# Performance work log

Hardware: AMD Instinct MI355X
Metric: run time of the kernel (lower is better)

## Reference

```python
import jax, jax.numpy as jnp
import numpy as np
from jax import lax

EPS = 1e-5
CARD = 32


def _bn(x, gamma, beta):
    # training-mode BatchNorm2d: batch statistics over (N, H, W) per channel
    mean = jnp.mean(x, axis=(0, 2, 3), keepdims=True)
    var = jnp.var(x, axis=(0, 2, 3), keepdims=True)
    inv = lax.rsqrt(var + EPS)
    return gamma[None, :, None, None] * (x - mean) * inv + beta[None, :, None, None]


def _conv(x, w, stride=1, padding='VALID', groups=1):
    return lax.conv_general_dilated(
        x, w, window_strides=(stride, stride), padding=padding,
        dimension_numbers=('NCHW', 'OIHW', 'NCHW'),
        feature_group_count=groups)


def setup_inputs() -> dict:
    key = jax.random.key(0)
    ks = jax.random.split(key, 4)
    N, Cin, H, W = 32, 256, 56, 56
    D, Cout = 16, 256
    CD = CARD * D  # 512
    x = jax.random.normal(ks[0], (N, Cin, H, W), dtype=jnp.float32)
    w1 = jax.random.normal(ks[1], (CD, Cin, 1, 1), dtype=jnp.float32) * 0.05
    w3 = jax.random.normal(ks[2], (CD, D, 3, 3), dtype=jnp.float32) * 0.05
    wa = jax.random.normal(ks[3], (Cout, CD, 1, 1), dtype=jnp.float32) * 0.05
    return {
        'x': x,
        'w1': w1, 'g1': jnp.ones(CD), 'b1': jnp.zeros(CD),
        'w3': w3, 'g3': jnp.ones(CD), 'b3': jnp.zeros(CD),
        'wa': wa, 'ga': jnp.ones(Cout), 'ba': jnp.zeros(Cout),
    }


def reference(x, w1, g1, b1, w3, g3, b3, wa, ga, ba):
    # 32 paths of (1x1 conv -> BN -> ReLU -> 3x3 conv -> BN -> ReLU) then concat
    # is exactly: one 1x1 conv to 512ch -> BN -> ReLU -> grouped 3x3 conv (32 groups)
    # -> BN -> ReLU  (per-channel BN commutes with channel concatenation).
    out = _conv(x, w1)                                   # [N, 512, H, W]
    out = jax.nn.relu(_bn(out, g1, b1))
    out = _conv(out, w3, stride=1, padding=((1, 1), (1, 1)), groups=CARD)
    out = jax.nn.relu(_bn(out, g3, b3))
    out = _conv(out, wa)                                 # [N, 256, H, W]
    out = _bn(out, ga, ba)
    out = out + x                                        # identity shortcut (stride=1, Cin==Cout)
    return jax.nn.relu(out)
```

## Files before the change

### kernel.cpp

```cpp
#include <hip/hip_runtime.h>

#define HW 3136
#define NPOS 100352.0f
#define NSLICE 32

typedef unsigned short ushortT;
typedef __attribute__((ext_vector_type(8))) short short8;
typedef __attribute__((ext_vector_type(4))) float floatx4;

__device__ inline float bf2f(ushortT u) {
    union { unsigned int i; float f; } v; v.i = ((unsigned int)u) << 16; return v.f;
}
__device__ inline ushortT f2bf(float f) {
    union { float f; unsigned int i; } v; v.f = f;
    unsigned int r = v.i + 0x7FFFu + ((v.i >> 16) & 1u);
    return (ushortT)(r >> 16);
}
__device__ inline unsigned int cvtpk(float lo, float hi) {
    unsigned int r;
    asm("v_cvt_pk_bf16_f32 %0, %1, %2" : "=v"(r) : "v"(lo), "v"(hi));
    return r;
}

__device__ inline void gl_lds16(const ushortT* g, ushortT* l) {
    __builtin_amdgcn_global_load_lds(
        (const __attribute__((address_space(1))) unsigned int*)g,
        (__attribute__((address_space(3))) unsigned int*)l, 16, 0, 0);
}

__global__ __launch_bounds__(256) void prep_k(const float* __restrict__ w1,
                                              const float* __restrict__ w3,
                                              const float* __restrict__ wa,
                                              ushortT* __restrict__ w1b,
                                              ushortT* __restrict__ wab,
                                              ushortT* __restrict__ w3b,
                                              float* __restrict__ partials) {
    int i = blockIdx.x * 256 + threadIdx.x;
    if (i < 131072) { w1b[i] = f2bf(w1[i]); wab[i] = f2bf(wa[i]); }
    if (i < 81920) {
        int ic = i & 15, oc = (i >> 4) & 15, rest = i >> 8;
        int s = rest % 10, g = rest / 10;
        w3b[i] = (s < 9) ? f2bf(w3[(((g * 16 + oc) * 16) + ic) * 9 + s]) : (ushortT)0;
        partials[i] = 0.f;
    }
}

__global__ __launch_bounds__(256) void transx_k(const float* __restrict__ x,
                                                ushortT* __restrict__ xb) {
    __shared__ float tf[64 * 65];
    const int t = threadIdx.x;
    const int p0 = blockIdx.x * 64, k0 = blockIdx.y * 64, n = blockIdx.z;
#pragma unroll
    for (int i = 0; i < 16; i++) {
        int idx = t + i * 256;
        int k = idx >> 6, p = idx & 63;
        tf[k * 65 + p] = x[((size_t)n * 256 + k0 + k) * HW + p0 + p];
    }
    __syncthreads();
#pragma unroll
    for (int i = 0; i < 2; i++) {
        int idx = t + i * 256;
        int p = idx >> 3, kq = (idx & 7) * 8;
        short8 o;
#pragma unroll
        for (int j = 0; j < 8; j++) o[j] = (short)f2bf(tf[(kq + j) * 65 + p]);
        *(short8*)&xb[((size_t)n * HW + p0 + p) * 256 + k0 + kq] = o;
    }
}

__global__ __launch_bounds__(512) void gemm1_k(const ushortT* __restrict__ xb,
                                               const ushortT* __restrict__ w1b,
                                               const float* __restrict__ zpad,
                                               ushortT* __restrict__ t1,
                                               float* __restrict__ p1) {
    __shared__ ushortT As[128 * 64];
    __shared__ ushortT Bs[256 * 64];
    const int t = threadIdx.x;
    const int P0 = blockIdx.x * 256, C0 = blockIdx.y * 128, n = blockIdx.z;
    const int w = t >> 6, lane = t & 63;
    const int mh = (w >> 2) * 64, nh = (w & 3) * 64;
    const int l15 = lane & 15, quad = lane >> 4;

    const int lrow = lane >> 3;
    const int slin = lane & 7;

    const ushortT* agp[2];
#pragma unroll
    for (int i = 0; i < 2; i++) {
        int row = w * 16 + lrow + i * 8;
        int sl = (slin ^ (row & 7)) * 8;
        agp[i] = w1b + (size_t)(C0 + row) * 256 + sl;
    }
    const ushortT* bgp[4];
#pragma unroll
    for (int i = 0; i < 4; i++) {
        int row = w * 32 + lrow + i * 8;
        int sl = (slin ^ (row & 7)) * 8;
        int p = P0 + row;
        bgp[i] = (p < HW) ? xb + ((size_t)n * HW + p) * 256 + sl
                          : (const ushortT*)zpad;
    }
    ushortT* al = As + (w * 16) * 64;
    ushortT* bl = Bs + (w * 32) * 64;

    floatx4 acc[4][4];
#pragma unroll
    for (int a = 0; a < 4; a++)
#pragma unroll
        for (int b = 0; b < 4; b++)
#pragma unroll
            for (int e = 0; e < 4; e++) acc[a][b][e] = 0.f;

    for (int kb = 0; kb < 256; kb += 64) {
#pragma unroll
        for (int i = 0; i < 2; i++) gl_lds16(agp[i] + kb, al + i * 512);
#pragma unroll
        for (int i = 0; i < 4; i++) gl_lds16(bgp[i] + kb, bl + i * 512);
        __syncthreads();
#pragma unroll
        for (int ks = 0; ks < 2; ks++) {
            short8 af[4], bfv[4];
#pragma unroll
            for (int mt = 0; mt < 4; mt++) {
                int row = mh + mt * 16 + l15, rx = row & 7;
                af[mt] = *(const short8*)&As[row * 64 + (((ks * 4 + quad) ^ rx) * 8)];
            }
#pragma unroll
            for (int nt = 0; nt < 4; nt++) {
                int row = nh + nt * 16 + l15, rx = row & 7;
                bfv[nt] = *(const short8*)&Bs[row * 64 + (((ks * 4 + quad) ^ rx) * 8)];
            }
#pragma unroll
            for (int mt = 0; mt < 4; mt++)
#pragma unroll
                for (int nt = 0; nt < 4; nt++)
                    acc[mt][nt] = __builtin_amdgcn_mfma_f32_16x16x32_bf16(
                        af[mt], bfv[nt], acc[mt][nt], 0, 0, 0);
        }
        __syncthreads();
    }
#pragma unroll
    for (int mt = 0; mt < 4; mt++) {
        int c = C0 + mh + mt * 16 + quad * 4;
#pragma unroll
        for (int nt = 0; nt < 4; nt++) {
            int pp = P0 + nh + nt * 16 + l15;
            if (pp < HW) {
                ushort4 o;
                o.x = f2bf(acc[mt][nt][0]); o.y = f2bf(acc[mt][nt][1]);
                o.z = f2bf(acc[mt][nt][2]); o.w = f2bf(acc[mt][nt][3]);
                *(ushort4*)&t1[((size_t)n * HW + pp) * 512 + c] = o;
            }
        }
    }
    float* ps = p1 + ((blockIdx.x + blockIdx.z * 13) & (NSLICE - 1)) * 1024;
#pragma unroll
    for (int mt = 0; mt < 4; mt++) {
        int c = C0 + mh + mt * 16 + quad * 4;
#pragma unroll
        for (int e = 0; e < 4; e++) {
            float sv = acc[mt][0][e] + acc[mt][1][e] + acc[mt][2][e] + acc[mt][3][e];
            float qv = acc[mt][0][e] * acc[mt][0][e] + acc[mt][1][e] * acc[mt][1][e]
                     + acc[mt][2][e] * acc[mt][2][e] + acc[mt][3][e] * acc[mt][3][e];
            sv += __shfl_xor(sv, 1); qv += __shfl_xor(qv, 1);
            sv += __shfl_xor(sv, 2); qv += __shfl_xor(qv, 2);
            sv += __shfl_xor(sv, 4); qv += __shfl_xor(qv, 4);
            sv += __shfl_xor(sv, 8); qv += __shfl_xor(qv, 8);
            if (l15 == 0) {
                atomicAdd(&ps[c + e], sv);
                atomicAdd(&ps[512 + c + e], qv);
            }
        }
    }
}

__global__ __launch_bounds__(256) void gconv_k(const ushortT* __restrict__ t1,
                                               const ushortT* __restrict__ w3b,
                                               const float* __restrict__ p1,
                                               const float* __restrict__ g1,
                                               const float* __restrict__ b1,
                                               ushortT* __restrict__ t2,
                                               float* __restrict__ p2) {
    __shared__ ushortT tile[8 * 590 * 8];
    __shared__ float scs[64], shs[64];
    const int t = threadIdx.x;
    const int rt = blockIdx.x, gg = blockIdx.y, n = blockIdx.z;
    const int r0 = rt * 8;

    if (t < 64) {
        int c = gg * 64 + t;
        float S = 0.f, Q = 0.f;
#pragma unroll
        for (int s = 0; s < NSLICE; s++) {
            S += p1[s * 1024 + c];
            Q += p1[s * 1024 + 512 + c];
        }
        float m = S * (1.f / NPOS);
        float var = Q * (1.f / NPOS) - m * m;
        float sc = g1[c] * rsqrtf(var + 1e-5f);
        scs[t] = sc; shs[t] = b1[c] - m * sc;
    }
    __syncthreads();

    const int chq = t & 7;
    float sc8[8], sh8[8];
#pragma unroll
    for (int j = 0; j < 8; j++) { sc8[j] = scs[chq * 8 + j]; sh8[j] = shs[chq * 8 + j]; }

    const ushortT* src = t1 + (size_t)n * HW * 512 + gg * 64 + chq * 8;
    short8 vreg[19];
#pragma unroll
    for (int i = 0; i < 19; i++) {
        int idx = t + i * 256;
        int pos = idx >> 3;
        int row = pos / 58, col = pos - row * 58;
        int ir = r0 - 1 + row, icl = col - 1;
        if (idx < 4640 && ir >= 0 && ir < 56 && icl >= 0 && icl < 56)
            vreg[i] = *(const short8*)&src[(size_t)(ir * 56 + icl) * 512];
    }
#pragma unroll
    for (int i = 0; i < 19; i++) {
        int idx = t + i * 256;
        if (idx >= 4640) continue;
        int pos = idx >> 3;
        int row = pos / 58, col = pos - row * 58;
        int ir = r0 - 1 + row, icl = col - 1;
        short8 o;
        if (ir >= 0 && ir < 56 && icl >= 0 && icl < 56) {
            float f[8];
#pragma unroll
            for (int j = 0; j < 8; j++)
                f[j] = fmaxf(fmaf(sc8[j], bf2f((ushortT)vreg[i][j]), sh8[j]), 0.f);
            union { short8 s; unsigned int u[4]; } ov;
#pragma unroll
            for (int j = 0; j < 4; j++) ov.u[j] = cvtpk(f[2 * j], f[2 * j + 1]);
            o = ov.s;
        } else {
#pragma unroll
            for (int j = 0; j < 8; j++) o[j] = 0;
        }
        *(short8*)&tile[((chq * 590) + row * 59 + col) * 8] = o;
    }
    __syncthreads();

    const int w = t >> 6, lane = t & 63;
    const int l15 = lane & 15, quad = lane >> 4;
    const int qh = quad >> 1, ql = quad & 1;
    const int g = gg * 4 + w;

    short8 af[5];
    int drv[5], dcv[5];
#pragma unroll
    for (int s = 0; s < 5; s++) {
        int shift = 2 * s + qh;
        af[s] = *(const short8*)&w3b[((g * 10 + shift) * 16 + l15) * 16 + ql * 8];
        if (shift == 9) shift = 8;
        drv[s] = shift / 3; dcv[s] = shift - drv[s] * 3;
    }

    const int pr = l15 >> 2, pc = l15 & 3;
    const int plane = (w * 2 + ql) * 590;
    float s4[4] = {0.f, 0.f, 0.f, 0.f}, q4[4] = {0.f, 0.f, 0.f, 0.f};

#pragma unroll
    for (int rh = 0; rh < 2; rh++) {
        const int rbase = rh * 4 + pr;
        floatx4 acc[14];
#pragma unroll
        for (int ct = 0; ct < 14; ct++)
#pragma unroll
            for (int e = 0; e < 4; e++) acc[ct][e] = 0.f;

#pragma unroll
        for (int ct = 0; ct < 14; ct++) {
            int colb = ct * 4 + pc;
#pragma unroll
            for (int s = 0; s < 5; s++) {
                short8 bfv = *(const short8*)&tile[(plane + (rbase + drv[s]) * 59 + colb + dcv[s]) * 8];
                acc[ct] = __builtin_amdgcn_mfma_f32_16x16x32_bf16(af[s], bfv, acc[ct], 0, 0, 0);
            }
        }
#pragma unroll
        for (int ct = 0; ct < 14; ct++) {
            int pos = (r0 + rh * 4 + pr) * 56 + ct * 4 + pc;
            ushort4 o;
            o.x = f2bf(acc[ct][0]); o.y = f2bf(acc[ct][1]);
            o.z = f2bf(acc[ct][2]); o.w = f2bf(acc[ct][3]);
            *(ushort4*)&t2[((size_t)n * HW + pos) * 512 + g * 16 + quad * 4] = o;
#pragma unroll
            for (int e = 0; e < 4; e++) {
                float a = acc[ct][e];
                s4[e] += a; q4[e] += a * a;
            }
        }
    }
    float* ps = p2 + ((blockIdx.x + blockIdx.z * 7) & (NSLICE - 1)) * 1024;
#pragma unroll
    for (int e = 0; e < 4; e++) {
        float sv = s4[e], qv = q4[e];
        sv += __shfl_xor(sv, 1); qv += __shfl_xor(qv, 1);
        sv += __shfl_xor(sv, 2); qv += __shfl_xor(qv, 2);
        sv += __shfl_xor(sv, 4); qv += __shfl_xor(qv, 4);
        sv += __shfl_xor(sv, 8); qv += __shfl_xor(qv, 8);
        if (l15 == 0) {
            atomicAdd(&ps[g * 16 + quad * 4 + e], sv);
            atomicAdd(&ps[512 + g * 16 + quad * 4 + e], qv);
        }
    }
}

__global__ __launch_bounds__(512) void gemm3_k(const ushortT* __restrict__ t2,
                                               const ushortT* __restrict__ wab,
                                               const float* __restrict__ p2,
                                               const float* __restrict__ g3,
                                               const float* __restrict__ b3,
                                               ushortT* __restrict__ t3,
                                               float* __restrict__ p3) {
    __shared__ ushortT As[256 * 64];
    __shared__ ushortT Bs[128 * 64];
    __shared__ float2 scsh[512];
    const int t = threadIdx.x;
    const int P0 = blockIdx.x * 128, n = blockIdx.y;
    const int w = t >> 6, lane = t & 63;
    const int mh = (w >> 1) * 64, nh = (w & 1) * 64;
    const int l15 = lane & 15, quad = lane >> 4;
    const int slin = t & 7;

    int brow[2]; const ushortT* bgp[2]; bool bval[2];
#pragma unroll
    for (int i = 0; i < 2; i++) {
        int row = (t >> 3) + i * 64;
        brow[i] = row;
        int p = P0 + row;
        bval[i] = (p < HW);
        int pe = bval[i] ? p : (HW - 1);
        bgp[i] = t2 + ((size_t)n * HW + pe) * 512 + slin * 8;
    }
    const int srow = w * 32 + (lane >> 3);
    const ushortT* agp[4];
#pragma unroll
    for (int i = 0; i < 4; i++) {
        int row = srow + i * 8;
        int sl = ((lane & 7) ^ (row & 7)) * 8;
        agp[i] = wab + (size_t)row * 512 + sl;
    }
    ushortT* al = As + (w * 32) * 64;

    short8 breg[2];
#pragma unroll
    for (int i = 0; i < 2; i++) breg[i] = *(const short8*)(bgp[i]);

    {
        int c = t;
        float S = 0.f, Q = 0.f;
#pragma unroll
        for (int s = 0; s < NSLICE; s++) {
            S += p2[s * 1024 + c];
            Q += p2[s * 1024 + 512 + c];
        }
        float m = S * (1.f / NPOS);
        float var = Q * (1.f / NPOS) - m * m;
        float sc = g3[c] * rsqrtf(var + 1e-5f);
        scsh[c] = make_float2(sc, b3[c] - m * sc);
    }
    __syncthreads();

    floatx4 acc[4][4];
#pragma unroll
    for (int a = 0; a < 4; a++)
#pragma unroll
        for (int b = 0; b < 4; b++)
#pragma unroll
            for (int e = 0; e < 4; e++) acc[a][b][e] = 0.f;

    for (int kb = 0; kb < 512; kb += 64) {
#pragma unroll
        for (int i = 0; i < 4; i++) gl_lds16(agp[i] + kb, al + i * 512);
#pragma unroll
        for (int i = 0; i < 2; i++) {
            int row = brow[i];
            ushortT* dst = Bs + row * 64 + ((slin ^ (row & 7)) * 8);
            if (bval[i]) {
                float f[8];
#pragma unroll
                for (int j = 0; j < 8; j++) {
                    float2 ss = scsh[kb + slin * 8 + j];
                    f[j] = fmaxf(fmaf(ss.x, bf2f((ushortT)breg[i][j]), ss.y), 0.f);
                }
                union { short8 s; unsigned int u[4]; } ov;
#pragma unroll
                for (int j = 0; j < 4; j++) ov.u[j] = cvtpk(f[2 * j], f[2 * j + 1]);
                *(short8*)dst = ov.s;
            } else {
                short8 z;
#pragma unroll
                for (int j = 0; j < 8; j++) z[j] = 0;
                *(short8*)dst = z;
            }
        }
        __syncthreads();
        int kbn = (kb + 64 < 512) ? kb + 64 : 0;
#pragma unroll
        for (int i = 0; i < 2; i++) breg[i] = *(const short8*)(bgp[i] + kbn);
#pragma unroll
        for (int ks = 0; ks < 2; ks++) {
            short8 af[4], bfv[4];
#pragma unroll
            for (int mt = 0; mt < 4; mt++) {
                int row = mh + mt * 16 + l15, rx = row & 7;
                af[mt] = *(const short8*)&As[row * 64 + (((ks * 4 + quad) ^ rx) * 8)];
            }
#pragma unroll
            for (int nt = 0; nt < 4; nt++) {
                int row = nh + nt * 16 + l15, rx = row & 7;
                bfv[nt] = *(const short8*)&Bs[row * 64 + (((ks * 4 + quad) ^ rx) * 8)];
            }
#pragma unroll
            for (int mt = 0; mt < 4; mt++)
#pragma unroll
                for (int nt = 0; nt < 4; nt++)
                    acc[mt][nt] = __builtin_amdgcn_mfma_f32_16x16x32_bf16(
                        af[mt], bfv[nt], acc[mt][nt], 0, 0, 0);
        }
        __syncthreads();
    }
#pragma unroll
    for (int mt = 0; mt < 4; mt++) {
        int c = mh + mt * 16 + quad * 4;
#pragma unroll
        for (int nt = 0; nt < 4; nt++) {
            int pp = P0 + nh + nt * 16 + l15;
            if (pp < HW) {
                uint2 o;
                o.x = cvtpk(acc[mt][nt][0], acc[mt][nt][1]);
                o.y = cvtpk(acc[mt][nt][2], acc[mt][nt][3]);
                *(uint2*)&t3[((size_t)n * HW + pp) * 256 + c] = o;
            }
        }
    }
    float* ps = p3 + ((blockIdx.x + blockIdx.y * 25) & (NSLICE - 1)) * 512;
#pragma unroll
    for (int mt = 0; mt < 4; mt++) {
        int c = mh + mt * 16 + quad * 4;
#pragma unroll
        for (int e = 0; e < 4; e++) {
            float sv = acc[mt][0][e] + acc[mt][1][e] + acc[mt][2][e] + acc[mt][3][e];
            float qv = acc[mt][0][e] * acc[mt][0][e] + acc[mt][1][e] * acc[mt][1][e]
                     + acc[mt][2][e] * acc[mt][2][e] + acc[mt][3][e] * acc[mt][3][e];
            sv += __shfl_xor(sv, 1); qv += __shfl_xor(qv, 1);
            sv += __shfl_xor(sv, 2); qv += __shfl_xor(qv, 2);
            sv += __shfl_xor(sv, 4); qv += __shfl_xor(qv, 4);
            sv += __shfl_xor(sv, 8); qv += __shfl_xor(qv, 8);
            if (l15 == 0) {
                atomicAdd(&ps[c + e], sv);
                atomicAdd(&ps[256 + c + e], qv);
            }
        }
    }
}

__global__ __launch_bounds__(256) void final_k(const ushortT* __restrict__ t3,
                                               const float* __restrict__ x,
                                               const float* __restrict__ p3,
                                               const float* __restrict__ ga,
                                               const float* __restrict__ ba,
                                               float* __restrict__ out) {
    __shared__ float tf[64 * 65];
    __shared__ float scs[64], shs[64];
    const int t = threadIdx.x;
    const int p0 = blockIdx.x * 64, c0 = blockIdx.y * 64, n = blockIdx.z;
    if (t < 64) {
        int c = c0 + t;
        float S = 0.f, Q = 0.f;
#pragma unroll
        for (int s = 0; s < NSLICE; s++) {
            S += p3[s * 512 + c];
            Q += p3[s * 512 + 256 + c];
        }
        float m = S * (1.f / NPOS);
        float var = Q * (1.f / NPOS) - m * m;
        float sc = ga[c] * rsqrtf(var + 1e-5f);
        scs[t] = sc; shs[t] = ba[c] - m * sc;
    }
    __syncthreads();
#pragma unroll
    for (int i = 0; i < 4; i++) {
        int idx = t + i * 256;
        int p = idx >> 4, cq = (idx & 15) * 4;
        ushort4 v = *(const ushort4*)&t3[((size_t)n * HW + p0 + p) * 256 + c0 + cq];
        tf[(cq + 0) * 65 + p] = fmaf(scs[cq + 0], bf2f(v.x), shs[cq + 0]);
        tf[(cq + 1) * 65 + p] = fmaf(scs[cq + 1], bf2f(v.y), shs[cq + 1]);
        tf[(cq + 2) * 65 + p] = fmaf(scs[cq + 2], bf2f(v.z), shs[cq + 2]);
        tf[(cq + 3) * 65 + p] = fmaf(scs[cq + 3], bf2f(v.w), shs[cq + 3]);
    }
    __syncthreads();
#pragma unroll
    for (int i = 0; i < 4; i++) {
        int idx = t + i * 256;
        int c = idx >> 4, pq = (idx & 15) * 4;
        size_t off = ((size_t)n * 256 + c0 + c) * HW + p0 + pq;
        float4 xv = *(const float4*)&x[off];
        float4 o;
        o.x = fmaxf(tf[c * 65 + pq + 0] + xv.x, 0.f);
        o.y = fmaxf(tf[c * 65 + pq + 1] + xv.y, 0.f);
        o.z = fmaxf(tf[c * 65 + pq + 2] + xv.z, 0.f);
        o.w = fmaxf(tf[c * 65 + pq + 3] + xv.w, 0.f);
        *(float4*)&out[off] = o;
    }
}

extern "C" void kernel_launch(void* const* d_in, const int* in_sizes, int n_in,
                              void* d_out, int out_size, void* d_ws, size_t ws_size,
                              hipStream_t stream) {
    const float* x  = (const float*)d_in[0];
    const float* w1 = (const float*)d_in[1];
    const float* g1 = (const float*)d_in[2];
    const float* b1 = (const float*)d_in[3];
    const float* w3 = (const float*)d_in[4];
    const float* g3 = (const float*)d_in[5];
    const float* b3 = (const float*)d_in[6];
    const float* wa = (const float*)d_in[7];
    const float* ga = (const float*)d_in[8];
    const float* ba = (const float*)d_in[9];
    float* out = (float*)d_out;

    char* ws = (char*)d_ws;
    ushortT* t1 = (ushortT*)ws;
    ushortT* t3 = t1;
    ushortT* xb = (ushortT*)(ws + 102760448);
    ushortT* t2 = (ushortT*)(ws + 102760448);
    ushortT* w1b = (ushortT*)(ws + 205520896);
    ushortT* wab = (ushortT*)(ws + 205783040);
    ushortT* w3b = (ushortT*)(ws + 206045184);
    float* partials = (float*)(ws + 206209024);
    float* pt1 = partials;
    float* pt2 = partials + 32 * 1024;
    float* pt3 = partials + 64 * 1024;

    prep_k<<<512, 256, 0, stream>>>(w1, w3, wa, w1b, wab, w3b, partials);
    transx_k<<<dim3(49, 4, 32), 256, 0, stream>>>(x, xb);
    gemm1_k<<<dim3(13, 4, 32), 512, 0, stream>>>(xb, w1b, pt3, t1, pt1);
    gconv_k<<<dim3(7, 8, 32), 256, 0, stream>>>(t1, w3b, pt1, g1, b1, t2, pt2);
    gemm3_k<<<dim3(25, 32), 512, 0, stream>>>(t2, wab, pt2, g3, b3, t3, pt3);
    final_k<<<dim3(49, 4, 32), 256, 0, stream>>>(t3, x, pt3, ga, ba, out);
}
```

Measured before the change: 424.1 us.

## Double-buffer LDS tiles in gemm1 with smaller K step to overlap loads

The first 1x1-conv GEMM kernel now keeps two LDS buffers with a K step of 32 instead of one buffer with a K step of 64. The global-to-LDS copy for the next slice is issued before the MFMA work on the current slice, so there is one barrier per iteration instead of two. The XOR swizzle is adapted to the 32-wide rows. In exchange the loop runs twice as many iterations with less MFMA work per barrier. The gl_lds writes to the next buffer may still need a wait before the barrier.

After: 434.0 us. +2.3%, slower.

```diff
diff --git a/kernel.cpp b/kernel.cpp
--- a/kernel.cpp
+++ b/kernel.cpp
@@ -73,35 +73,32 @@
                                                const float* __restrict__ zpad,
                                                ushortT* __restrict__ t1,
                                                float* __restrict__ p1) {
-    __shared__ ushortT As[128 * 64];
-    __shared__ ushortT Bs[256 * 64];
+    __shared__ ushortT As[2][128 * 32];
+    __shared__ ushortT Bs[2][256 * 32];
     const int t = threadIdx.x;
     const int P0 = blockIdx.x * 256, C0 = blockIdx.y * 128, n = blockIdx.z;
     const int w = t >> 6, lane = t & 63;
     const int mh = (w >> 2) * 64, nh = (w & 3) * 64;
     const int l15 = lane & 15, quad = lane >> 4;
 
-    const int lrow = lane >> 3;
-    const int slin = lane & 7;
-
-    const ushortT* agp[2];
+    const int lrow = lane >> 2;
+    const int slin = lane & 3;
+
+    const ushortT* agp;
+    {
+        int row = w * 16 + lrow;
+        int sl = (slin ^ ((row >> 1) & 3)) * 8;
+        agp = w1b + (size_t)(C0 + row) * 256 + sl;
+    }
+    const ushortT* bgp[2];
 #pragma unroll
     for (int i = 0; i < 2; i++) {
-        int row = w * 16 + lrow + i * 8;
-        int sl = (slin ^ (row & 7)) * 8;
-        agp[i] = w1b + (size_t)(C0 + row) * 256 + sl;
-    }
-    const ushortT* bgp[4];
-#pragma unroll
-    for (int i = 0; i < 4; i++) {
-        int row = w * 32 + lrow + i * 8;
-        int sl = (slin ^ (row & 7)) * 8;
+        int row = w * 32 + i * 16 + lrow;
+        int sl = (slin ^ ((row >> 1) & 3)) * 8;
         int p = P0 + row;
         bgp[i] = (p < HW) ? xb + ((size_t)n * HW + p) * 256 + sl
                           : (const ushortT*)zpad;
     }
-    ushortT* al = As + (w * 16) * 64;
-    ushortT* bl = Bs + (w * 32) * 64;
 
     floatx4 acc[4][4];
 #pragma unroll
@@ -111,32 +108,36 @@
 #pragma unroll
             for (int e = 0; e < 4; e++) acc[a][b][e] = 0.f;
 
-    for (int kb = 0; kb < 256; kb += 64) {
-#pragma unroll
-        for (int i = 0; i < 2; i++) gl_lds16(agp[i] + kb, al + i * 512);
-#pragma unroll
-        for (int i = 0; i < 4; i++) gl_lds16(bgp[i] + kb, bl + i * 512);
-        __syncthreads();
-#pragma unroll
-        for (int ks = 0; ks < 2; ks++) {
-            short8 af[4], bfv[4];
-#pragma unroll
-            for (int mt = 0; mt < 4; mt++) {
-                int row = mh + mt * 16 + l15, rx = row & 7;
-                af[mt] = *(const short8*)&As[row * 64 + (((ks * 4 + quad) ^ rx) * 8)];
-            }
-#pragma unroll
-            for (int nt = 0; nt < 4; nt++) {
-                int row = nh + nt * 16 + l15, rx = row & 7;
-                bfv[nt] = *(const short8*)&Bs[row * 64 + (((ks * 4 + quad) ^ rx) * 8)];
-            }
-#pragma unroll
-            for (int mt = 0; mt < 4; mt++)
-#pragma unroll
-                for (int nt = 0; nt < 4; nt++)
-                    acc[mt][nt] = __builtin_amdgcn_mfma_f32_16x16x32_bf16(
-                        af[mt], bfv[nt], acc[mt][nt], 0, 0, 0);
-        }
+    gl_lds16(agp, &As[0][(w * 16) * 32]);
+    gl_lds16(bgp[0], &Bs[0][(w * 32) * 32]);
+    gl_lds16(bgp[1], &Bs[0][(w * 32 + 16) * 32]);
+    __syncthreads();
+
+    for (int tt = 0; tt < 8; tt++) {
+        const int cur = tt & 1;
+        if (tt < 7) {
+            const int kb = (tt + 1) * 32, nb = cur ^ 1;
+            gl_lds16(agp + kb, &As[nb][(w * 16) * 32]);
+            gl_lds16(bgp[0] + kb, &Bs[nb][(w * 32) * 32]);
+            gl_lds16(bgp[1] + kb, &Bs[nb][(w * 32 + 16) * 32]);
+        }
+        short8 af[4], bfv[4];
+#pragma unroll
+        for (int mt = 0; mt < 4; mt++) {
+            int row = mh + mt * 16 + l15, rx = (row >> 1) & 3;
+            af[mt] = *(const short8*)&As[cur][row * 32 + ((quad ^ rx) * 8)];
+        }
+#pragma unroll
+        for (int nt = 0; nt < 4; nt++) {
+            int row = nh + nt * 16 + l15, rx = (row >> 1) & 3;
+            bfv[nt] = *(const short8*)&Bs[cur][row * 32 + ((quad ^ rx) * 8)];
+        }
+#pragma unroll
+        for (int mt = 0; mt < 4; mt++)
+#pragma unroll
+            for (int nt = 0; nt < 4; nt++)
+                acc[mt][nt] = __builtin_amdgcn_mfma_f32_16x16x32_bf16(
+                    af[mt], bfv[nt], acc[mt][nt], 0, 0, 0);
         __syncthreads();
     }
 #pragma unroll
```

## Restructure gemm1 to load full K into LDS with smaller tiles and swizzled grid

Applied to the files above, without the earlier changes.

The 1x1-conv GEMM now stages the whole K=256 slice of both operands into LDS at once, with warp-specialized loading (half the waves load weights, half load activations). This removes the K-loop and its per-step barriers. The position tile shrinks from 256 to 128 and the grid becomes a 1D launch of 3200 blocks, remapped so that consecutive blocks share input tiles across channel blocks for better L2 reuse. The cost is 128 KB of LDS per block, which limits occupancy to one block per CU, and there is no overlap between loading and MFMA compute.

Measured after the change: 452.3 us. 6.6% more time.

```diff
diff --git a/kernel.cpp b/kernel.cpp
--- a/kernel.cpp
+++ b/kernel.cpp
@@ -73,77 +73,90 @@
                                                const float* __restrict__ zpad,
                                                ushortT* __restrict__ t1,
                                                float* __restrict__ p1) {
-    __shared__ ushortT As[128 * 64];
-    __shared__ ushortT Bs[256 * 64];
+    __shared__ ushortT As[128 * 256];
+    __shared__ ushortT Bs[128 * 256];
     const int t = threadIdx.x;
-    const int P0 = blockIdx.x * 256, C0 = blockIdx.y * 128, n = blockIdx.z;
+    const int bid = blockIdx.x;
+    const int sb = bid >> 5, u = bid & 31;
+    const int pt = sb * 8 + (u & 7);
+    const int yq = u >> 3;
+    const int px = pt % 25, pz = pt / 25;
+    const int P0 = px * 128, C0 = yq * 128, n = pz;
+
     const int w = t >> 6, lane = t & 63;
-    const int mh = (w >> 2) * 64, nh = (w & 3) * 64;
+    const int mh = (w >> 2) * 64, nh = (w & 3) * 32;
     const int l15 = lane & 15, quad = lane >> 4;
 
-    const int lrow = lane >> 3;
-    const int slin = lane & 7;
-
-    const ushortT* agp[2];
-#pragma unroll
-    for (int i = 0; i < 2; i++) {
-        int row = w * 16 + lrow + i * 8;
-        int sl = (slin ^ (row & 7)) * 8;
-        agp[i] = w1b + (size_t)(C0 + row) * 256 + sl;
-    }
-    const ushortT* bgp[4];
-#pragma unroll
-    for (int i = 0; i < 4; i++) {
-        int row = w * 32 + lrow + i * 8;
-        int sl = (slin ^ (row & 7)) * 8;
-        int p = P0 + row;
-        bgp[i] = (p < HW) ? xb + ((size_t)n * HW + p) * 256 + sl
-                          : (const ushortT*)zpad;
-    }
-    ushortT* al = As + (w * 16) * 64;
-    ushortT* bl = Bs + (w * 32) * 64;
-
-    floatx4 acc[4][4];
+    const int lrow = lane >> 5;
+    const int slin = lane & 31;
+    if (w < 4) {
+        ushortT* dst = As + (w * 32) * 256;
+        const ushortT* gp[4];
+#pragma unroll
+        for (int j = 0; j < 4; j++) {
+            int row = w * 32 + j * 2 + lrow;
+            int sl = (slin ^ (row & 7)) * 8;
+            gp[j] = w1b + (size_t)(C0 + row) * 256 + sl;
+        }
+#pragma unroll
+        for (int i4 = 0; i4 < 4; i4++)
+#pragma unroll
+            for (int j = 0; j < 4; j++)
+                gl_lds16(gp[j] + (size_t)i4 * 8 * 256, dst + (i4 * 8 + j * 2) * 256);
+    } else {
+        const int w2 = w - 4;
+        ushortT* dst = Bs + (w2 * 32) * 256;
+#pragma unroll
+        for (int i4 = 0; i4 < 4; i4++)
+#pragma unroll
+            for (int j = 0; j < 4; j++) {
+                int row = w2 * 32 + i4 * 8 + j * 2 + lrow;
+                int sl = (slin ^ (row & 7)) * 8;
+                int p = P0 + row;
+                const ushortT* src = (p < HW)
+                    ? xb + ((size_t)n * HW + p) * 256 + sl
+                    : (const ushortT*)zpad + sl;
+                gl_lds16(src, dst + (i4 * 8 + j * 2) * 256);
+            }
+    }
+
+    floatx4 acc[4][2];
 #pragma unroll
     for (int a = 0; a < 4; a++)
 #pragma unroll
-        for (int b = 0; b < 4; b++)
+        for (int b = 0; b < 2; b++)
 #pragma unroll
             for (int e = 0; e < 4; e++) acc[a][b][e] = 0.f;
 
-    for (int kb = 0; kb < 256; kb += 64) {
-#pragma unroll
-        for (int i = 0; i < 2; i++) gl_lds16(agp[i] + kb, al + i * 512);
-#pragma unroll
-        for (int i = 0; i < 4; i++) gl_lds16(bgp[i] + kb, bl + i * 512);
-        __syncthreads();
-#pragma unroll
-        for (int ks = 0; ks < 2; ks++) {
-            short8 af[4], bfv[4];
-#pragma unroll
-            for (int mt = 0; mt < 4; mt++) {
-                int row = mh + mt * 16 + l15, rx = row & 7;
-                af[mt] = *(const short8*)&As[row * 64 + (((ks * 4 + quad) ^ rx) * 8)];
-            }
-#pragma unroll
-            for (int nt = 0; nt < 4; nt++) {
-                int row = nh + nt * 16 + l15, rx = row & 7;
-                bfv[nt] = *(const short8*)&Bs[row * 64 + (((ks * 4 + quad) ^ rx) * 8)];
-            }
-#pragma unroll
-            for (int mt = 0; mt < 4; mt++)
-#pragma unroll
-                for (int nt = 0; nt < 4; nt++)
-                    acc[mt][nt] = __builtin_amdgcn_mfma_f32_16x16x32_bf16(
-                        af[mt], bfv[nt], acc[mt][nt], 0, 0, 0);
-        }
-        __syncthreads();
-    }
+    __syncthreads();
+
+#pragma unroll
+    for (int ks = 0; ks < 8; ks++) {
+        const int slot = ks * 4 + quad;
+        short8 af[4], bfv[2];
+#pragma unroll
+        for (int mt = 0; mt < 4; mt++) {
+            int row = mh + mt * 16 + l15;
+            af[mt] = *(const short8*)&As[row * 256 + ((slot ^ (row & 7)) * 8)];
+        }
+#pragma unroll
+        for (int nt = 0; nt < 2; nt++) {
+            int row = nh + nt * 16 + l15;
+            bfv[nt] = *(const short8*)&Bs[row * 256 + ((slot ^ (row & 7)) * 8)];
+        }
+#pragma unroll
+        for (int mt = 0; mt < 4; mt++)
+#pragma unroll
+            for (int nt = 0; nt < 2; nt++)
+                acc[mt][nt] = __builtin_amdgcn_mfma_f32_16x16x32_bf16(
+                    af[mt], bfv[nt], acc[mt][nt], 0, 0, 0);
+    }
+
 #pragma unroll
     for (int mt = 0; mt < 4; mt++) {
         int c = C0 + mh + mt * 16 + quad * 4;
 #pragma unroll
-        for (int nt = 0; nt < 4; nt++) {
+        for (int nt = 0; nt < 2; nt++) {
             int pp = P0 + nh + nt * 16 + l15;
             if (pp < HW) {
                 ushort4 o;
@@ -153,15 +166,14 @@
             }
         }
     }
-    float* ps = p1 + ((blockIdx.x + blockIdx.z * 13) & (NSLICE - 1)) * 1024;
+    float* ps = p1 + ((px + pz * 25) & (NSLICE - 1)) * 1024;
 #pragma unroll
     for (int mt = 0; mt < 4; mt++) {
         int c = C0 + mh + mt * 16 + quad * 4;
 #pragma unroll
         for (int e = 0; e < 4; e++) {
-            float sv = acc[mt][0][e] + acc[mt][1][e] + acc[mt][2][e] + acc[mt][3][e];
-            float qv = acc[mt][0][e] * acc[mt][0][e] + acc[mt][1][e] * acc[mt][1][e]
-                     + acc[mt][2][e] * acc[mt][2][e] + acc[mt][3][e] * acc[mt][3][e];
+            float sv = acc[mt][0][e] + acc[mt][1][e];
+            float qv = acc[mt][0][e] * acc[mt][0][e] + acc[mt][1][e] * acc[mt][1][e];
             sv += __shfl_xor(sv, 1); qv += __shfl_xor(qv, 1);
             sv += __shfl_xor(sv, 2); qv += __shfl_xor(qv, 2);
             sv += __shfl_xor(sv, 4); qv += __shfl_xor(qv, 4);
@@ -539,7 +551,7 @@
 
     prep_k<<<512, 256, 0, stream>>>(w1, w3, wa, w1b, wab, w3b, partials);
     transx_k<<<dim3(49, 4, 32), 256, 0, stream>>>(x, xb);
-    gemm1_k<<<dim3(13, 4, 32), 512, 0, stream>>>(xb, w1b, pt3, t1, pt1);
+    gemm1_k<<<3200, 512, 0, stream>>>(xb, w1b, pt3, t1, pt1);
     gconv_k<<<dim3(7, 8, 32), 256, 0, stream>>>(t1, w3b, pt1, g1, b1, t2, pt2);
     gemm3_k<<<dim3(25, 32), 512, 0, stream>>>(t2, wab, pt2, g3, b3, t3, pt3);
     final_k<<<dim3(49, 4, 32), 256, 0, stream>>>(t3, x, pt3, ga, ba, out);
```
